# Performance work log

Hardware: AMD Instinct MI355X
Metric: run time of the kernel (lower is better)

## Reference

```python
import jax, jax.numpy as jnp
import numpy as np

R = 32          # voxel resolution
EPS_BN = 1e-4   # BatchNorm eps (module uses eps=0.0001)
NEG = 0.1       # LeakyReLU slope


def voxelize_avg(features, coords, r):
    """PVCNN cube voxelization: normalize coords to [0,r-1], scatter-mean features.
    Returns avg voxel grid [b,c,r,r,r], per-point flat voxel index [b,n] (int32),
    and float normalized coords [b,3,n] used for trilinear devoxelization."""
    b, c, n = features.shape
    norm = coords - coords.mean(axis=2, keepdims=True)
    scale = jnp.max(jnp.sqrt(jnp.sum(norm * norm, axis=1, keepdims=True)),
                    axis=2, keepdims=True) * 2.0  # normalize=True, eps=0
    norm = norm / scale + 0.5
    norm = jnp.clip(norm * r, 0.0, r - 1.0)                  # [b,3,n]
    vox = jnp.round(norm).astype(jnp.int32)
    inds = (vox[:, 0] * r + vox[:, 1]) * r + vox[:, 2]       # [b,n]
    seg = (inds + jnp.arange(b, dtype=jnp.int32)[:, None] * (r ** 3)).reshape(-1)
    feat = features.transpose(0, 2, 1).reshape(b * n, c)
    sums = jax.ops.segment_sum(feat, seg, num_segments=b * r ** 3)
    cnt = jax.ops.segment_sum(jnp.ones((b * n,), features.dtype), seg,
                              num_segments=b * r ** 3)
    avg = sums / jnp.maximum(cnt, 1.0)[:, None]
    avg = avg.reshape(b, r ** 3, c).transpose(0, 2, 1)       # [b,c,r^3]
    return avg.reshape(b, c, r, r, r), inds, norm


def trilinear_devox(vox, norm_coords, r):
    """F.trilinear_devoxelize: gather 8 corner voxels per point, blend trilinearly."""
    b, c = vox.shape[:2]
    f = vox.reshape(b, c, r ** 3)
    xyz0 = jnp.floor(norm_coords)
    frac = norm_coords - xyz0                                 # [b,3,n]
    i0 = xyz0.astype(jnp.int32)
    i1 = jnp.minimum(i0 + 1, r - 1)
    out = jnp.zeros((b, c, norm_coords.shape[2]), vox.dtype)
    for dx in (0, 1):
        for dy in (0, 1):
            for dz in (0, 1):
                ix = i1[:, 0] if dx else i0[:, 0]
                iy = i1[:, 1] if dy else i0[:, 1]
                iz = i1[:, 2] if dz else i0[:, 2]
                w = ((frac[:, 0] if dx else 1.0 - frac[:, 0]) *
                     (frac[:, 1] if dy else 1.0 - frac[:, 1]) *
                     (frac[:, 2] if dz else 1.0 - frac[:, 2]))  # [b,n]
                idx = (ix * r + iy) * r + iz
                out = out + jnp.take_along_axis(f, idx[:, None, :], axis=2) * w[:, None, :]
    return out


def conv3d(x, w, b):
    y = jax.lax.conv_general_dilated(x, w, (1, 1, 1), 'SAME',
                                     dimension_numbers=('NCDHW', 'OIDHW', 'NCDHW'))
    return y + b[None, :, None, None, None]


def bn_affine(x, g, b):
    # inference-mode BatchNorm with running mean 0 / var 1
    shape = (1, -1) + (1,) * (x.ndim - 2)
    return x * (g / jnp.sqrt(1.0 + EPS_BN)).reshape(shape) + b.reshape(shape)


def setup_inputs() -> dict:
    key = jax.random.key(0)
    ks = jax.random.split(key, 6)
    B, C, N, O = 8, 32, 65536, 32
    return {
        'features': jax.random.normal(ks[0], (B, C, N), jnp.float32),
        'coords':   jax.random.normal(ks[1], (B, 3, N), jnp.float32),
        'conv1_w':  jax.random.normal(ks[2], (O, C, 3, 3, 3), jnp.float32) * 0.05,
        'conv1_b':  jnp.zeros((O,), jnp.float32),
        'bn1_g':    jnp.ones((O,), jnp.float32),
        'bn1_b':    jnp.zeros((O,), jnp.float32),
        'conv2_w':  jax.random.normal(ks[3], (O, O, 3, 3, 3), jnp.float32) * 0.05,
        'conv2_b':  jnp.zeros((O,), jnp.float32),
        'bn2_g':    jnp.ones((O,), jnp.float32),
        'bn2_b':    jnp.zeros((O,), jnp.float32),
        'point_w':  jax.random.normal(ks[4], (O, 2 * C), jnp.float32) * 0.05,
        'point_b':  jnp.zeros((O,), jnp.float32),
        'pbn_g':    jnp.ones((O,), jnp.float32),
        'pbn_b':    jnp.zeros((O,), jnp.float32),
    }


def reference(features, coords, conv1_w, conv1_b, bn1_g, bn1_b,
              conv2_w, conv2_b, bn2_g, bn2_b,
              point_w, point_b, pbn_g, pbn_b):
    b, c, n = features.shape
    avg, inds, norm_coords = voxelize_avg(features, coords, R)
    # voxel branch: Conv3d-BN-LeakyReLU x2, then trilinear devoxelize back to points
    h = jax.nn.leaky_relu(bn_affine(conv3d(avg, conv1_w, conv1_b), bn1_g, bn1_b), NEG)
    h = jax.nn.leaky_relu(bn_affine(conv3d(h, conv2_w, conv2_b), bn2_g, bn2_b), NEG)
    voxel_features = trilinear_devox(h, norm_coords, R)       # [b,out,n]
    # dgcnn point kernel: gather each point's voxel-average, subtract, concat
    avg_flat = avg.reshape(b, c, R ** 3)
    center = jnp.take_along_axis(avg_flat, inds[:, None, :], axis=2)  # [b,c,n]
    related = features - center   # cube voxelization: inds never -1, mask is all False
    point_in = jnp.concatenate([related, features], axis=1)   # [b,2c,n]
    pf = jnp.einsum('oc,bcn->bon', point_w, point_in) + point_b[None, :, None]
    point_features = jax.nn.relu(bn_affine(pf, pbn_g, pbn_b))
    return voxel_features + point_features                    # fused_features [b,out,n]
```

## Files before the change

kernel.cpp:

```cpp
#include <hip/hip_runtime.h>

#define BATCH 8
#define CH 32
#define NPTS 65536
#define OCH 32
#define RES 32
#define R3 32768

#define OF_MEAN  0
#define OF_SCALE 32
#define OF_B1F   64
#define OF_B2F   96
#define OF_PBF   128
#define OF_WT1   1024
#define OF_WT2   28672
#define OF_PWF   56320
#define OF_INDS  65536
#define OF_SLOT  (OF_INDS + 524288)
#define OF_LIST  (OF_SLOT + 524288)
#define OF_CNT   (OF_LIST + 524288)
#define OF_START (OF_CNT + 262144)
#define OF_BLKSUM (OF_START + 262144)
#define OF_AVG   (OF_BLKSUM + 4096)
#define OF_H1    (OF_AVG + 8388608)
#define OF_H2    (OF_H1 + 8388608)
#define OF_FT    OF_H1

__global__ void k_prep(const float* __restrict__ c1w, const float* __restrict__ c1b,
                       const float* __restrict__ g1,  const float* __restrict__ bb1,
                       const float* __restrict__ c2w, const float* __restrict__ c2b,
                       const float* __restrict__ g2,  const float* __restrict__ bb2,
                       const float* __restrict__ pw,  const float* __restrict__ pb,
                       const float* __restrict__ gp,  const float* __restrict__ bbp,
                       float* __restrict__ ws) {
    int tid = threadIdx.x;
    float sq = sqrtf(1.0f + 1e-4f);
    for (int i = tid; i < 27648; i += 256) {
        int tap = i >> 10; int rem = i & 1023; int o = rem >> 5; int c = rem & 31;
        ws[OF_WT1 + i] = c1w[(o * 32 + c) * 27 + tap] * (g1[o] / sq);
        ws[OF_WT2 + i] = c2w[(o * 32 + c) * 27 + tap] * (g2[o] / sq);
    }
    for (int i = tid; i < 2048; i += 256) {
        int o = i >> 6;
        ws[OF_PWF + i] = pw[i] * (gp[o] / sq);
    }
    if (tid < 32) {
        ws[OF_B1F + tid] = c1b[tid] * (g1[tid] / sq) + bb1[tid];
        ws[OF_B2F + tid] = c2b[tid] * (g2[tid] / sq) + bb2[tid];
        ws[OF_PBF + tid] = pb[tid] * (gp[tid] / sq) + bbp[tid];
    }
}

__global__ void k_mean(const float* __restrict__ coords, float* __restrict__ ws) {
    __shared__ double sd[256];
    int ba = blockIdx.x;
    const float* p = coords + (size_t)ba * NPTS;
    double acc = 0.0;
    for (int i = threadIdx.x; i < NPTS; i += 256) acc += (double)p[i];
    sd[threadIdx.x] = acc; __syncthreads();
    for (int s = 128; s > 0; s >>= 1) {
        if (threadIdx.x < s) sd[threadIdx.x] += sd[threadIdx.x + s];
        __syncthreads();
    }
    if (threadIdx.x == 0) ws[OF_MEAN + ba] = (float)(sd[0] / (double)NPTS);
}

__global__ void k_scale(const float* __restrict__ coords, float* __restrict__ ws) {
    __shared__ float sd[256];
    int b = blockIdx.x;
    float mx = ws[OF_MEAN + b * 3 + 0];
    float my = ws[OF_MEAN + b * 3 + 1];
    float mz = ws[OF_MEAN + b * 3 + 2];
    const float* px = coords + (size_t)(b * 3 + 0) * NPTS;
    const float* py = coords + (size_t)(b * 3 + 1) * NPTS;
    const float* pz = coords + (size_t)(b * 3 + 2) * NPTS;
    float m = 0.0f;
    for (int i = threadIdx.x; i < NPTS; i += 256) {
        float dx = px[i] - mx, dy = py[i] - my, dz = pz[i] - mz;
        float s = __fadd_rn(__fadd_rn(__fmul_rn(dx, dx), __fmul_rn(dy, dy)), __fmul_rn(dz, dz));
        m = fmaxf(m, s);
    }
    sd[threadIdx.x] = m; __syncthreads();
    for (int s = 128; s > 0; s >>= 1) {
        if (threadIdx.x < s) sd[threadIdx.x] = fmaxf(sd[threadIdx.x], sd[threadIdx.x + s]);
        __syncthreads();
    }
    if (threadIdx.x == 0) ws[OF_SCALE + b] = 2.0f * sqrtf(sd[0]);
}

__global__ __launch_bounds__(256) void k_transpose(const float* __restrict__ f,
                                                   float* __restrict__ ws) {
    __shared__ float t[32][65];
    int blk = blockIdx.x;
    int b = blk >> 10;
    int p0 = (blk & 1023) << 6;
    int tid = threadIdx.x;
    #pragma unroll
    for (int it = 0; it < 8; ++it) {
        int e = it * 256 + tid; int c = e >> 6; int pp = e & 63;
        t[c][pp] = f[(size_t)(((b << 5) + c) << 16) + p0 + pp];
    }
    __syncthreads();
    #pragma unroll
    for (int it = 0; it < 8; ++it) {
        int e = it * 256 + tid; int pp = e >> 5; int c = e & 31;
        ws[OF_FT + ((size_t)((b << 16) + p0 + pp) << 5) + c] = t[c][pp];
    }
}

__global__ __launch_bounds__(256) void k_voxassign(const float* __restrict__ coords,
                                                   float* __restrict__ ws) {
    int gid = blockIdx.x * 256 + threadIdx.x;
    int b = gid >> 16, p = gid & 65535;
    float sc = ws[OF_SCALE + b];
    int vox[3];
    #pragma unroll
    for (int a = 0; a < 3; ++a) {
        float val = coords[(size_t)((b * 3 + a) << 16) + p];
        float m = ws[OF_MEAN + b * 3 + a];
        float v = (val - m) / sc + 0.5f;
        v = v * 32.0f;
        v = fminf(fmaxf(v, 0.0f), 31.0f);
        vox[a] = (int)rintf(v);
    }
    int vb = (b << 15) + ((vox[0] * 32 + vox[1]) * 32 + vox[2]);
    int* wsi = (int*)ws;
    wsi[OF_INDS + gid] = vb;
    int slot = atomicAdd(wsi + OF_CNT + vb, 1);
    wsi[OF_SLOT + gid] = slot;
}

__global__ void k_scanA(float* __restrict__ ws) {
    __shared__ int s[256];
    int tid = threadIdx.x;
    const int* cnt = (const int*)ws + OF_CNT;
    s[tid] = cnt[blockIdx.x * 256 + tid];
    __syncthreads();
    for (int st = 128; st > 0; st >>= 1) {
        if (tid < st) s[tid] += s[tid + st];
        __syncthreads();
    }
    if (tid == 0) ((int*)ws)[OF_BLKSUM + blockIdx.x] = s[0];
}

__global__ void k_scanB(float* __restrict__ ws) {
    __shared__ int s[1024];
    int tid = threadIdx.x;
    int* bs = (int*)ws + OF_BLKSUM;
    int v = bs[tid];
    s[tid] = v; __syncthreads();
    for (int off = 1; off < 1024; off <<= 1) {
        int x = (tid >= off) ? s[tid - off] : 0;
        __syncthreads();
        s[tid] += x;
        __syncthreads();
    }
    bs[tid] = s[tid] - v;
}

__global__ void k_scanC(float* __restrict__ ws) {
    __shared__ int s[256];
    int tid = threadIdx.x;
    int gid = blockIdx.x * 256 + tid;
    int v = ((const int*)ws)[OF_CNT + gid];
    s[tid] = v; __syncthreads();
    for (int off = 1; off < 256; off <<= 1) {
        int x = (tid >= off) ? s[tid - off] : 0;
        __syncthreads();
        s[tid] += x;
        __syncthreads();
    }
    ((int*)ws)[OF_START + gid] = ((const int*)ws)[OF_BLKSUM + blockIdx.x] + s[tid] - v;
}

__global__ __launch_bounds__(256) void k_scatter(float* __restrict__ ws) {
    int gid = blockIdx.x * 256 + threadIdx.x;
    int* wsi = (int*)ws;
    int vb = wsi[OF_INDS + gid];
    int slot = wsi[OF_SLOT + gid];
    wsi[OF_LIST + wsi[OF_START + vb] + slot] = gid;
}

__global__ __launch_bounds__(256) void k_sum(float* __restrict__ ws) {
    int t = blockIdx.x * 256 + threadIdx.x;
    int vb = t >> 6;
    int lane = t & 63;
    int half = lane >> 5, c = lane & 31;
    const int* wsi = (const int*)ws;
    int n = wsi[OF_CNT + vb];
    int s0 = wsi[OF_START + vb];
    const int* list = (const int*)ws + OF_LIST;
    float acc = 0.0f;
    for (int j = half; j < n; j += 2) {
        int pt = list[s0 + j];
        acc += ws[OF_FT + ((size_t)pt << 5) + c];
    }
    acc += __shfl_xor(acc, 32, 64);
    if (half == 0)
        ws[OF_AVG + ((size_t)vb << 5) + c] = acc / fmaxf((float)n, 1.0f);
}

__global__ __launch_bounds__(256) void k_conv(const float* __restrict__ in,
                                              float* __restrict__ out,
                                              const float* __restrict__ wT,
                                              const float* __restrict__ bias) {
    int t = blockIdx.x * 256 + threadIdx.x;
    int b = t >> 15, v = t & 32767;
    int x = v >> 10, y = (v >> 5) & 31, z = v & 31;
    float acc[32];
    #pragma unroll
    for (int o = 0; o < 32; ++o) acc[o] = 0.0f;

    #pragma unroll 1
    for (int kd = 0; kd < 3; ++kd) {
        #pragma unroll 1
        for (int kh = 0; kh < 3; ++kh) {
            #pragma unroll 1
            for (int kw = 0; kw < 3; ++kw) {
                int xx = x + kd - 1, yy = y + kh - 1, zz = z + kw - 1;
                bool ok = ((unsigned)xx < 32u) & ((unsigned)yy < 32u) & ((unsigned)zz < 32u);
                if (ok) {
                    const float* ip = in + ((size_t)((b << 15) + ((xx << 10) + (yy << 5) + zz)) << 5);
                    float iv[32];
                    #pragma unroll
                    for (int k = 0; k < 8; ++k)
                        *(float4*)(iv + 4 * k) = ((const float4*)ip)[k];
                    int tap = (kd * 3 + kh) * 3 + kw;
                    const float* wp = wT + tap * 1024;
                    #pragma unroll
                    for (int o = 0; o < 32; ++o) {
                        float a = acc[o];
                        #pragma unroll
                        for (int c = 0; c < 32; ++c)
                            a = fmaf(iv[c], wp[o * 32 + c], a);
                        acc[o] = a;
                    }
                }
            }
        }
    }
    float* op = out + ((size_t)t << 5);
    #pragma unroll
    for (int o = 0; o < 32; ++o) {
        float yv = acc[o] + bias[o];
        op[o] = yv >= 0.0f ? yv : 0.1f * yv;
    }
}

__global__ __launch_bounds__(256) void k_final(const float* __restrict__ features,
                                               const float* __restrict__ coords,
                                               float* __restrict__ out,
                                               const float* __restrict__ ws) {
    int gid = blockIdx.x * 256 + threadIdx.x;
    int b = gid >> 16, p = gid & 65535;
    const int* wsi = (const int*)ws;
    int vb = wsi[OF_INDS + gid];
    const float* av = ws + OF_AVG + ((size_t)vb << 5);
    float cen[32];
    #pragma unroll
    for (int k = 0; k < 8; ++k) *(float4*)(cen + 4 * k) = ((const float4*)av)[k];
    float xin[64];
    #pragma unroll
    for (int c = 0; c < 32; ++c) {
        float f = features[(size_t)(((b << 5) + c) << 16) + p];
        xin[c] = f - cen[c];
        xin[32 + c] = f;
    }
    float pacc[32];
    const float* pwp = ws + OF_PWF;
    #pragma unroll
    for (int o = 0; o < 32; ++o) {
        float a = ws[OF_PBF + o];
        #pragma unroll
        for (int cc = 0; cc < 64; ++cc)
            a = fmaf(xin[cc], pwp[o * 64 + cc], a);
        pacc[o] = fmaxf(a, 0.0f);
    }
    float sc = ws[OF_SCALE + b];
    float vxyz[3];
    #pragma unroll
    for (int a = 0; a < 3; ++a) {
        float val = coords[(size_t)((b * 3 + a) << 16) + p];
        float m = ws[OF_MEAN + b * 3 + a];
        float v = (val - m) / sc + 0.5f;
        v = v * 32.0f;
        v = fminf(fmaxf(v, 0.0f), 31.0f);
        vxyz[a] = v;
    }
    float x0 = floorf(vxyz[0]), y0 = floorf(vxyz[1]), z0 = floorf(vxyz[2]);
    float tx = vxyz[0] - x0, ty = vxyz[1] - y0, tz = vxyz[2] - z0;
    int ix0 = (int)x0, iy0 = (int)y0, iz0 = (int)z0;
    int ix1 = min(ix0 + 1, 31), iy1 = min(iy0 + 1, 31), iz1 = min(iz0 + 1, 31);
    const float* h2 = ws + OF_H2 + (((size_t)b << 15) << 5);
    #pragma unroll
    for (int dx = 0; dx < 2; ++dx)
    #pragma unroll
    for (int dy = 0; dy < 2; ++dy)
    #pragma unroll
    for (int dz = 0; dz < 2; ++dz) {
        int idx = ((dx ? ix1 : ix0) * 32 + (dy ? iy1 : iy0)) * 32 + (dz ? iz1 : iz0);
        float w8 = (dx ? tx : 1.0f - tx) * (dy ? ty : 1.0f - ty) * (dz ? tz : 1.0f - tz);
        const float* hp = h2 + ((size_t)idx << 5);
        float hv[32];
        #pragma unroll
        for (int k = 0; k < 8; ++k) *(float4*)(hv + 4 * k) = ((const float4*)hp)[k];
        #pragma unroll
        for (int o = 0; o < 32; ++o) pacc[o] = fmaf(w8, hv[o], pacc[o]);
    }
    #pragma unroll
    for (int o = 0; o < 32; ++o)
        out[(size_t)(((b << 5) + o) << 16) + p] = pacc[o];
}

extern "C" void kernel_launch(void* const* d_in, const int* in_sizes, int n_in,
                              void* d_out, int out_size, void* d_ws, size_t ws_size,
                              hipStream_t stream) {
    const float* features = (const float*)d_in[0];
    const float* coords   = (const float*)d_in[1];
    const float* c1w = (const float*)d_in[2];
    const float* c1b = (const float*)d_in[3];
    const float* g1  = (const float*)d_in[4];
    const float* bb1 = (const float*)d_in[5];
    const float* c2w = (const float*)d_in[6];
    const float* c2b = (const float*)d_in[7];
    const float* g2  = (const float*)d_in[8];
    const float* bb2 = (const float*)d_in[9];
    const float* pw  = (const float*)d_in[10];
    const float* pb  = (const float*)d_in[11];
    const float* gp  = (const float*)d_in[12];
    const float* bbp = (const float*)d_in[13];
    float* ws  = (float*)d_ws;
    float* out = (float*)d_out;

    hipLaunchKernelGGL(k_prep, dim3(1), dim3(256), 0, stream,
                       c1w, c1b, g1, bb1, c2w, c2b, g2, bb2, pw, pb, gp, bbp, ws);
    hipMemsetAsync(ws + OF_CNT, 0, (size_t)262144 * sizeof(int), stream);
    hipLaunchKernelGGL(k_mean, dim3(24), dim3(256), 0, stream, coords, ws);
    hipLaunchKernelGGL(k_scale, dim3(8), dim3(256), 0, stream, coords, ws);
    hipLaunchKernelGGL(k_transpose, dim3(8192), dim3(256), 0, stream, features, ws);
    hipLaunchKernelGGL(k_voxassign, dim3(2048), dim3(256), 0, stream, coords, ws);
    hipLaunchKernelGGL(k_scanA, dim3(1024), dim3(256), 0, stream, ws);
    hipLaunchKernelGGL(k_scanB, dim3(1), dim3(1024), 0, stream, ws);
    hipLaunchKernelGGL(k_scanC, dim3(1024), dim3(256), 0, stream, ws);
    hipLaunchKernelGGL(k_scatter, dim3(2048), dim3(256), 0, stream, ws);
    hipLaunchKernelGGL(k_sum, dim3(65536), dim3(256), 0, stream, ws);
    hipLaunchKernelGGL(k_conv, dim3(1024), dim3(256), 0, stream,
                       ws + OF_AVG, ws + OF_H1, ws + OF_WT1, ws + OF_B1F);
    hipLaunchKernelGGL(k_conv, dim3(1024), dim3(256), 0, stream,
                       ws + OF_H1, ws + OF_H2, ws + OF_WT2, ws + OF_B2F);
    hipLaunchKernelGGL(k_final, dim3(2048), dim3(256), 0, stream, features, coords, out, ws);
}
```

Baseline: 1.175 ms.

## Remap conv3d threads to output-channel lanes over 16-voxel z-strips

The 3x3x3 conv kernel previously had each thread compute all 32 output channels for one voxel, reading the weights through a uniform per-thread path. Now each wave handles 16 consecutive z voxels: each lane owns one output channel and half the input channels, keeps its 16 weights per tap in registers, and accumulates 16 voxels. The two channel halves are combined with a cross-lane shuffle. This cuts weight traffic and register pressure and quadruples the grid, at the cost of redundant input loads across lanes (the same addresses per half-wave, which should be served from cache).

Result: slower. 2.994 ms (+154.9%).

```diff
diff --git a/kernel.cpp b/kernel.cpp
--- a/kernel.cpp
+++ b/kernel.cpp
@@ -204,46 +204,68 @@
                                               float* __restrict__ out,
                                               const float* __restrict__ wT,
                                               const float* __restrict__ bias) {
-    int t = blockIdx.x * 256 + threadIdx.x;
-    int b = t >> 15, v = t & 32767;
-    int x = v >> 10, y = (v >> 5) & 31, z = v & 31;
-    float acc[32];
-    #pragma unroll
-    for (int o = 0; o < 32; ++o) acc[o] = 0.0f;
+    int tid = threadIdx.x;
+    int wave = __builtin_amdgcn_readfirstlane(tid >> 6);
+    int lane = tid & 63;
+    int o = lane & 31;
+    int ch = lane >> 5;
+    int vbase = (blockIdx.x * 4 + wave) * 16;
+    int b = vbase >> 15, v0 = vbase & 32767;
+    int x = v0 >> 10, y = (v0 >> 5) & 31, z0 = v0 & 31;
+
+    float acc[16];
+    #pragma unroll
+    for (int v = 0; v < 16; ++v) acc[v] = 0.0f;
+
+    const float* wlane = wT + o * 32 + ch * 16;
 
     #pragma unroll 1
     for (int kd = 0; kd < 3; ++kd) {
+        int xx = x + kd - 1;
+        if ((unsigned)xx >= 32u) continue;
         #pragma unroll 1
         for (int kh = 0; kh < 3; ++kh) {
-            #pragma unroll 1
+            int yy = y + kh - 1;
+            if ((unsigned)yy >= 32u) continue;
+            const float* plane = in + ((size_t)((b << 15) + (xx << 10) + (yy << 5)) << 5) + ch * 16;
+            #pragma unroll
             for (int kw = 0; kw < 3; ++kw) {
-                int xx = x + kd - 1, yy = y + kh - 1, zz = z + kw - 1;
-                bool ok = ((unsigned)xx < 32u) & ((unsigned)yy < 32u) & ((unsigned)zz < 32u);
-                if (ok) {
-                    const float* ip = in + ((size_t)((b << 15) + ((xx << 10) + (yy << 5) + zz)) << 5);
-                    float iv[32];
-                    #pragma unroll
-                    for (int k = 0; k < 8; ++k)
-                        *(float4*)(iv + 4 * k) = ((const float4*)ip)[k];
-                    int tap = (kd * 3 + kh) * 3 + kw;
-                    const float* wp = wT + tap * 1024;
-                    #pragma unroll
-                    for (int o = 0; o < 32; ++o) {
-                        float a = acc[o];
-                        #pragma unroll
-                        for (int c = 0; c < 32; ++c)
-                            a = fmaf(iv[c], wp[o * 32 + c], a);
-                        acc[o] = a;
+                const float* wp = wlane + ((kd * 3 + kh) * 3 + kw) * 1024;
+                float4 w0 = ((const float4*)wp)[0];
+                float4 w1 = ((const float4*)wp)[1];
+                float4 w2 = ((const float4*)wp)[2];
+                float4 w3 = ((const float4*)wp)[3];
+                int zoff = z0 + kw - 1;
+                const float* ip0 = plane + (ptrdiff_t)zoff * 32;
+                #pragma unroll
+                for (int v = 0; v < 16; ++v) {
+                    int zz = zoff + v;
+                    if ((unsigned)zz < 32u) {
+                        const float4* ip = (const float4*)(ip0 + v * 32);
+                        float4 i0 = ip[0], i1 = ip[1], i2 = ip[2], i3 = ip[3];
+                        float a = acc[v];
+                        a = fmaf(i0.x, w0.x, a); a = fmaf(i0.y, w0.y, a);
+                        a = fmaf(i0.z, w0.z, a); a = fmaf(i0.w, w0.w, a);
+                        a = fmaf(i1.x, w1.x, a); a = fmaf(i1.y, w1.y, a);
+                        a = fmaf(i1.z, w1.z, a); a = fmaf(i1.w, w1.w, a);
+                        a = fmaf(i2.x, w2.x, a); a = fmaf(i2.y, w2.y, a);
+                        a = fmaf(i2.z, w2.z, a); a = fmaf(i2.w, w2.w, a);
+                        a = fmaf(i3.x, w3.x, a); a = fmaf(i3.y, w3.y, a);
+                        a = fmaf(i3.z, w3.z, a); a = fmaf(i3.w, w3.w, a);
+                        acc[v] = a;
                     }
                 }
             }
         }
     }
-    float* op = out + ((size_t)t << 5);
-    #pragma unroll
-    for (int o = 0; o < 32; ++o) {
-        float yv = acc[o] + bias[o];
-        op[o] = yv >= 0.0f ? yv : 0.1f * yv;
+    float bo = bias[o];
+    #pragma unroll
+    for (int v = 0; v < 16; ++v) {
+        float tot = acc[v] + __shfl_xor(acc[v], 32, 64);
+        if (ch == 0) {
+            float yv = tot + bo;
+            out[((size_t)(vbase + v) << 5) + o] = yv >= 0.0f ? yv : 0.1f * yv;
+        }
     }
 }
 
@@ -344,9 +366,9 @@
     hipLaunchKernelGGL(k_scanC, dim3(1024), dim3(256), 0, stream, ws);
     hipLaunchKernelGGL(k_scatter, dim3(2048), dim3(256), 0, stream, ws);
     hipLaunchKernelGGL(k_sum, dim3(65536), dim3(256), 0, stream, ws);
-    hipLaunchKernelGGL(k_conv, dim3(1024), dim3(256), 0, stream,
+    hipLaunchKernelGGL(k_conv, dim3(4096), dim3(256), 0, stream,
                        ws + OF_AVG, ws + OF_H1, ws + OF_WT1, ws + OF_B1F);
-    hipLaunchKernelGGL(k_conv, dim3(1024), dim3(256), 0, stream,
+    hipLaunchKernelGGL(k_conv, dim3(4096), dim3(256), 0, stream,
                        ws + OF_H1, ws + OF_H2, ws + OF_WT2, ws + OF_B2F);
     hipLaunchKernelGGL(k_final, dim3(2048), dim3(256), 0, stream, features, coords, out, ws);
 }
```
